# Optimization experiments

Hardware: AMD Instinct MI355X
Metric: run time of the kernel (lower is better)

The kernel has to match this reference:

```python
import jax, jax.numpy as jnp
import numpy as np

NEAR = 0.01          # near_lidar
FAR = 0.81           # far_lidar
DENSITY_SCALE = 1.0
ACTIVE_SENSOR = False
WEIGHT_THRESH = 1e-4  # mask = weights > 0.0001
N_RAYS, N_STEPS, N_SEM, N_ATTR = 8192, 768, 20, 2


def setup_inputs() -> dict:
    key = jax.random.key(0)
    k1, k2, k3 = jax.random.split(key, 3)
    # sigma scaled so alphas span opaque->transparent (realistic density field)
    sigma = jax.random.uniform(k1, (N_RAYS, N_STEPS), dtype=jnp.float32) * 30.0
    sigma_semantic = jax.random.normal(k2, (N_RAYS, N_STEPS, N_SEM), dtype=jnp.float32)
    attr = jax.random.uniform(k3, (N_RAYS, N_STEPS, N_ATTR), dtype=jnp.float32)
    return {"sigma": sigma, "sigma_semantic": sigma_semantic, "attr": attr}


def reference(sigma, sigma_semantic, attr):
    N, S = sigma.shape
    # z_vals: identical for all rays (nears/fars are constants), no perturb
    z_vals = NEAR + (FAR - NEAR) * jnp.linspace(0.0, 1.0, S, dtype=sigma.dtype)[None, :]  # [1,S]
    sample_dist = (FAR - NEAR) / S
    deltas = jnp.concatenate(
        [z_vals[..., 1:] - z_vals[..., :-1],
         jnp.full_like(z_vals[..., :1], sample_dist)], axis=-1)  # [1,S]
    scale = 2.0 if ACTIVE_SENSOR else 1.0
    alphas = 1.0 - jnp.exp(-scale * deltas * DENSITY_SCALE * sigma)  # [N,S]
    # transmittance via shifted cumprod: T_i = prod_{j<i} (1 - a_j + 1e-15)
    trans = jnp.cumprod(
        jnp.concatenate([jnp.ones((N, 1), sigma.dtype), 1.0 - alphas + 1e-15], axis=-1),
        axis=-1)[..., :-1]
    weights = alphas * trans  # [N,S]
    # attribute() is evaluated only where weights > threshold; elsewhere contributes 0
    mask = (weights > WEIGHT_THRESH)[..., None]
    attr_m = jnp.where(mask, attr, 0.0)
    weights_sum = weights.sum(axis=-1)                      # [N]
    depth = (weights * z_vals).sum(axis=-1)                 # [N]
    semantic = jnp.einsum('ns,nsk->nk', weights, sigma_semantic)  # [N,20]
    image = jnp.einsum('ns,nsa->na', weights, attr_m)             # [N,2]
    image = jnp.concatenate([image, semantic], axis=-1)     # use_semantic=True -> [N,22]
    # pack depth_lidar, image_lidar, weights_sum_lidar into one array [N, 24]
    return jnp.concatenate([depth[:, None], image, weights_sum[:, None]], axis=-1)
```

## Files before the change

### kernel.cpp

```cpp
#include <hip/hip_runtime.h>


#define NSTEPS 768
#define NSEM 20
#define NOUT 24

static constexpr float kNear = 0.01f;
static constexpr float kFar  = 0.81f;
static constexpr float kWThresh = 1e-4f;

__global__ __launch_bounds__(256) void lidar_render_kernel(
    const float* __restrict__ sigma,
    const float* __restrict__ sem,
    const float* __restrict__ attr,
    float* __restrict__ out)
{
    const int ray  = blockIdx.x;
    const int t    = threadIdx.x;
    const int lane = t & 63;
    const int wave = t >> 6;

    __shared__ float w_lds[NSTEPS];
    __shared__ float wave_tot[4];
    __shared__ float red[4][NOUT];

    const float h  = (kFar - kNear) / (float)(NSTEPS - 1);
    const float h2 = (kFar - kNear) / (float)NSTEPS;
    const float zstep = (kFar - kNear) / (float)(NSTEPS - 1);

    const int s0 = 3 * t;
    const float* sp = sigma + (size_t)ray * NSTEPS + s0;
    float sg0 = sp[0], sg1 = sp[1], sg2 = sp[2];
    float x0 = h * sg0;
    float x1 = h * sg1;
    float x2 = ((s0 + 2) == (NSTEPS - 1) ? h2 : h) * sg2;
    float local = x0 + x1 + x2;

    float inc = local;
    #pragma unroll
    for (int d = 1; d < 64; d <<= 1) {
        float v = __shfl_up(inc, d, 64);
        if (lane >= d) inc += v;
    }
    if (lane == 63) wave_tot[wave] = inc;
    __syncthreads();
    float base = inc - local;
    #pragma unroll
    for (int wv = 0; wv < 4; ++wv)
        if (wv < wave) base += wave_tot[wv];

    float T  = __expf(-base);
    float e0 = __expf(-x0), e1 = __expf(-x1), e2 = __expf(-x2);
    float w0 = T * (1.0f - e0);  T *= e0;
    float w1 = T * (1.0f - e1);  T *= e1;
    float w2 = T * (1.0f - e2);

    w_lds[s0]     = w0;
    w_lds[s0 + 1] = w1;
    w_lds[s0 + 2] = w2;

    const float z0 = kNear + zstep * (float)s0;
    float depth_p = w0 * z0 + w1 * (z0 + zstep) + w2 * (z0 + 2.0f * zstep);
    float wsum_p  = w0 + w1 + w2;
    __syncthreads();

    float acc_sem[NSEM];
    #pragma unroll
    for (int k = 0; k < NSEM; ++k) acc_sem[k] = 0.0f;
    float acc_im0 = 0.0f, acc_im1 = 0.0f;

    const float* semp = sem  + (size_t)ray * NSTEPS * NSEM;
    const float* attp = attr + (size_t)ray * NSTEPS * 2;

    #pragma unroll
    for (int i = 0; i < 3; ++i) {
        const int s = t + 256 * i;
        const float w = w_lds[s];
        const float4* p4 = (const float4*)(semp + (size_t)s * NSEM);
        #pragma unroll
        for (int j = 0; j < 5; ++j) {
            float4 v = p4[j];
            acc_sem[4 * j + 0] += w * v.x;
            acc_sem[4 * j + 1] += w * v.y;
            acc_sem[4 * j + 2] += w * v.z;
            acc_sem[4 * j + 3] += w * v.w;
        }
        float2 a2 = *(const float2*)(attp + (size_t)s * 2);
        if (w > kWThresh) {
            acc_im0 += w * a2.x;
            acc_im1 += w * a2.y;
        }
    }

    float vals[NOUT];
    vals[0] = depth_p;
    vals[1] = acc_im0;
    vals[2] = acc_im1;
    #pragma unroll
    for (int k = 0; k < NSEM; ++k) vals[3 + k] = acc_sem[k];
    vals[23] = wsum_p;

    #pragma unroll
    for (int j = 0; j < NOUT; ++j) {
        float v = vals[j];
        #pragma unroll
        for (int d = 32; d >= 1; d >>= 1) v += __shfl_xor(v, d, 64);
        vals[j] = v;
    }
    if (lane == 0) {
        #pragma unroll
        for (int j = 0; j < NOUT; ++j) red[wave][j] = vals[j];
    }
    __syncthreads();
    if (t < NOUT) {
        out[(size_t)ray * NOUT + t] = red[0][t] + red[1][t] + red[2][t] + red[3][t];
    }
}

extern "C" void kernel_launch(void* const* d_in, const int* in_sizes, int n_in,
                              void* d_out, int out_size, void* d_ws, size_t ws_size,
                              hipStream_t stream) {
    const float* sigma = (const float*)d_in[0];
    const float* sem   = (const float*)d_in[1];
    const float* attr  = (const float*)d_in[2];
    float* out = (float*)d_out;

    const int n_rays = in_sizes[0] / NSTEPS;
    lidar_render_kernel<<<n_rays, 256, 0, stream>>>(sigma, sem, attr, out);
}
```

Measured before the change: 672.6 us.

## Coalesce semantic loads with a 320-thread block and LDS cross-thread reduction

```diff
diff --git a/kernel.cpp b/kernel.cpp
--- a/kernel.cpp
+++ b/kernel.cpp
@@ -4,12 +4,13 @@
 #define NSTEPS 768
 #define NSEM 20
 #define NOUT 24
+#define BLK 320
 
 static constexpr float kNear = 0.01f;
 static constexpr float kFar  = 0.81f;
 static constexpr float kWThresh = 1e-4f;
 
-__global__ __launch_bounds__(256) void lidar_render_kernel(
+__global__ __launch_bounds__(BLK) void lidar_render_kernel(
     const float* __restrict__ sigma,
     const float* __restrict__ sem,
     const float* __restrict__ attr,
@@ -22,98 +23,118 @@
 
     __shared__ float w_lds[NSTEPS];
     __shared__ float wave_tot[4];
-    __shared__ float red[4][NOUT];
+    __shared__ float acc_lds[BLK * 4];
+    __shared__ float red_d[5], red_w[5], red_i0[5], red_i1[5];
+
+    const float* sp = sigma + (size_t)ray * NSTEPS;
+    #pragma unroll
+    for (int j = 0; j < 3; ++j) {
+        int idx = t + BLK * j;
+        if (idx < NSTEPS) w_lds[idx] = sp[idx];
+    }
+    __syncthreads();
 
     const float h  = (kFar - kNear) / (float)(NSTEPS - 1);
     const float h2 = (kFar - kNear) / (float)NSTEPS;
-    const float zstep = (kFar - kNear) / (float)(NSTEPS - 1);
 
-    const int s0 = 3 * t;
-    const float* sp = sigma + (size_t)ray * NSTEPS + s0;
-    float sg0 = sp[0], sg1 = sp[1], sg2 = sp[2];
-    float x0 = h * sg0;
-    float x1 = h * sg1;
-    float x2 = ((s0 + 2) == (NSTEPS - 1) ? h2 : h) * sg2;
-    float local = x0 + x1 + x2;
-
-    float inc = local;
-    #pragma unroll
-    for (int d = 1; d < 64; d <<= 1) {
-        float v = __shfl_up(inc, d, 64);
-        if (lane >= d) inc += v;
+    float x0 = 0.f, x1 = 0.f, x2 = 0.f, local = 0.f, inc = 0.f;
+    if (t < 256) {
+        float sg0 = w_lds[3 * t], sg1 = w_lds[3 * t + 1], sg2 = w_lds[3 * t + 2];
+        x0 = h * sg0;
+        x1 = h * sg1;
+        x2 = ((3 * t + 2) == (NSTEPS - 1) ? h2 : h) * sg2;
+        local = x0 + x1 + x2;
+        inc = local;
+        #pragma unroll
+        for (int d = 1; d < 64; d <<= 1) {
+            float v = __shfl_up(inc, d, 64);
+            if (lane >= d) inc += v;
+        }
+        if (lane == 63) wave_tot[wave] = inc;
     }
-    if (lane == 63) wave_tot[wave] = inc;
-    __syncthreads();
-    float base = inc - local;
-    #pragma unroll
-    for (int wv = 0; wv < 4; ++wv)
-        if (wv < wave) base += wave_tot[wv];
-
-    float T  = __expf(-base);
-    float e0 = __expf(-x0), e1 = __expf(-x1), e2 = __expf(-x2);
-    float w0 = T * (1.0f - e0);  T *= e0;
-    float w1 = T * (1.0f - e1);  T *= e1;
-    float w2 = T * (1.0f - e2);
-
-    w_lds[s0]     = w0;
-    w_lds[s0 + 1] = w1;
-    w_lds[s0 + 2] = w2;
-
-    const float z0 = kNear + zstep * (float)s0;
-    float depth_p = w0 * z0 + w1 * (z0 + zstep) + w2 * (z0 + 2.0f * zstep);
-    float wsum_p  = w0 + w1 + w2;
     __syncthreads();
 
-    float acc_sem[NSEM];
+    float depth_p = 0.f, wsum_p = 0.f;
+    if (t < 256) {
+        float base = inc - local;
+        #pragma unroll
+        for (int wv = 0; wv < 4; ++wv)
+            if (wv < wave) base += wave_tot[wv];
+        float T  = __expf(-base);
+        float e0 = __expf(-x0), e1 = __expf(-x1), e2 = __expf(-x2);
+        float w0 = T * (1.0f - e0);  T *= e0;
+        float w1 = T * (1.0f - e1);  T *= e1;
+        float w2 = T * (1.0f - e2);
+        w_lds[3 * t]     = w0;
+        w_lds[3 * t + 1] = w1;
+        w_lds[3 * t + 2] = w2;
+        const float z0 = kNear + h * (float)(3 * t);
+        depth_p = w0 * z0 + w1 * (z0 + h) + w2 * (z0 + 2.0f * h);
+        wsum_p  = w0 + w1 + w2;
+    }
+    __syncthreads();
+
+    const int sbase = t / 5;
+    const float4* p4 = (const float4*)(sem + (size_t)ray * NSTEPS * NSEM) + t;
+    float a0 = 0.f, a1 = 0.f, a2 = 0.f, a3 = 0.f;
     #pragma unroll
-    for (int k = 0; k < NSEM; ++k) acc_sem[k] = 0.0f;
-    float acc_im0 = 0.0f, acc_im1 = 0.0f;
+    for (int k = 0; k < 12; ++k) {
+        float4 v = p4[(size_t)BLK * k];
+        float w = w_lds[sbase + 64 * k];
+        a0 += w * v.x; a1 += w * v.y; a2 += w * v.z; a3 += w * v.w;
+    }
+    acc_lds[t * 4 + 0] = a0;
+    acc_lds[t * 4 + 1] = a1;
+    acc_lds[t * 4 + 2] = a2;
+    acc_lds[t * 4 + 3] = a3;
 
-    const float* semp = sem  + (size_t)ray * NSTEPS * NSEM;
-    const float* attp = attr + (size_t)ray * NSTEPS * 2;
-
+    const float4* a4 = (const float4*)(attr + (size_t)ray * NSTEPS * 2);
+    float ai0 = 0.f, ai1 = 0.f;
     #pragma unroll
-    for (int i = 0; i < 3; ++i) {
-        const int s = t + 256 * i;
-        const float w = w_lds[s];
-        const float4* p4 = (const float4*)(semp + (size_t)s * NSEM);
-        #pragma unroll
-        for (int j = 0; j < 5; ++j) {
-            float4 v = p4[j];
-            acc_sem[4 * j + 0] += w * v.x;
-            acc_sem[4 * j + 1] += w * v.y;
-            acc_sem[4 * j + 2] += w * v.z;
-            acc_sem[4 * j + 3] += w * v.w;
-        }
-        float2 a2 = *(const float2*)(attp + (size_t)s * 2);
-        if (w > kWThresh) {
-            acc_im0 += w * a2.x;
-            acc_im1 += w * a2.y;
+    for (int k = 0; k < 2; ++k) {
+        int p = t + BLK * k;
+        if (p < (NSTEPS * 2) / 4) {
+            float4 v = a4[p];
+            float wA = w_lds[2 * p], wB = w_lds[2 * p + 1];
+            if (wA > kWThresh) { ai0 += wA * v.x; ai1 += wA * v.y; }
+            if (wB > kWThresh) { ai0 += wB * v.z; ai1 += wB * v.w; }
         }
     }
 
-    float vals[NOUT];
-    vals[0] = depth_p;
-    vals[1] = acc_im0;
-    vals[2] = acc_im1;
+    float dv = depth_p, wvs = wsum_p, i0 = ai0, i1 = ai1;
     #pragma unroll
-    for (int k = 0; k < NSEM; ++k) vals[3 + k] = acc_sem[k];
-    vals[23] = wsum_p;
-
-    #pragma unroll
-    for (int j = 0; j < NOUT; ++j) {
-        float v = vals[j];
-        #pragma unroll
-        for (int d = 32; d >= 1; d >>= 1) v += __shfl_xor(v, d, 64);
-        vals[j] = v;
+    for (int d = 32; d >= 1; d >>= 1) {
+        dv  += __shfl_xor(dv,  d, 64);
+        wvs += __shfl_xor(wvs, d, 64);
+        i0  += __shfl_xor(i0,  d, 64);
+        i1  += __shfl_xor(i1,  d, 64);
     }
     if (lane == 0) {
-        #pragma unroll
-        for (int j = 0; j < NOUT; ++j) red[wave][j] = vals[j];
+        red_d[wave]  = dv;
+        red_w[wave]  = wvs;
+        red_i0[wave] = i0;
+        red_i1[wave] = i1;
     }
     __syncthreads();
+
     if (t < NOUT) {
-        out[(size_t)ray * NOUT + t] = red[0][t] + red[1][t] + red[2][t] + red[3][t];
+        float r;
+        if (t == 0) {
+            r = red_d[0] + red_d[1] + red_d[2] + red_d[3] + red_d[4];
+        } else if (t == 1) {
+            r = red_i0[0] + red_i0[1] + red_i0[2] + red_i0[3] + red_i0[4];
+        } else if (t == 2) {
+            r = red_i1[0] + red_i1[1] + red_i1[2] + red_i1[3] + red_i1[4];
+        } else if (t == 23) {
+            r = red_w[0] + red_w[1] + red_w[2] + red_w[3] + red_w[4];
+        } else {
+            const int c = t - 3;
+            r = 0.f;
+            #pragma unroll 8
+            for (int m = 0; m < 64; ++m)
+                r += acc_lds[20 * m + c];
+        }
+        out[(size_t)ray * NOUT + t] = r;
     }
 }
 
@@ -126,5 +147,5 @@
     float* out = (float*)d_out;
 
     const int n_rays = in_sizes[0] / NSTEPS;
-    lidar_render_kernel<<<n_rays, 256, 0, stream>>>(sigma, sem, attr, out);
+    lidar_render_kernel<<<n_rays, BLK, 0, stream>>>(sigma, sem, attr, out);
 }
```

Result: no change. 675.9 us (+0.5%).
